# Performance work log

Measured on AMD Instinct MI355X. Metric: run time of the kernel, lower is better.

Reference implementation:

```python
import jax, jax.numpy as jnp
import numpy as np

H = 160; W = 160          # BEV grid
C = 256                   # embed_dims
NH = 8                    # num_heads
HD = C // NH              # head dim
NP = 4                    # num_points
LC = 2                    # max_num_levels == num agents for cross attn
Q = H * W                 # num queries = num values per level
EPS = 1e-5

def _lin(key, din, dout):
    k1, k2 = jax.random.split(key)
    s = float(1.0 / np.sqrt(din))
    return (jax.random.uniform(k1, (din, dout), jnp.float32, -s, s),
            jax.random.uniform(k2, (dout,), jnp.float32, -s, s))

def setup_inputs():
    ks = jax.random.split(jax.random.key(0), 16)
    inp = {
        "query": jax.random.normal(ks[0], (1, Q, C), jnp.float32),
        "query_pos": jax.random.normal(ks[1], (1, Q, C), jnp.float32),
        "value": jax.random.normal(ks[2], (LC, Q, C), jnp.float32),
        "ref_2d": jax.random.uniform(ks[3], (1, Q, LC, 2), jnp.float32),
        "spatial_shapes": jnp.full((LC, 2), H, dtype=jnp.int32),
    }
    i = 4
    for pre, L in (("sa", 1), ("ca", LC)):
        inp[pre + "_off_w"], inp[pre + "_off_b"] = _lin(ks[i], C, L * NH * NP * 2); i += 1
        inp[pre + "_aw_w"], inp[pre + "_aw_b"] = _lin(ks[i], C, L * NH * NP); i += 1
        inp[pre + "_vp_w"], inp[pre + "_vp_b"] = _lin(ks[i], C, C); i += 1
        inp[pre + "_op_w"], inp[pre + "_op_b"] = _lin(ks[i], C, C); i += 1
    inp["ffn_w1"], inp["ffn_b1"] = _lin(ks[i], C, 4 * C); i += 1
    inp["ffn_w2"], inp["ffn_b2"] = _lin(ks[i], 4 * C, C); i += 1
    for j in (1, 2, 3):
        inp["ln%d_g" % j] = jnp.ones((C,), jnp.float32)
        inp["ln%d_b" % j] = jnp.zeros((C,), jnp.float32)
    return inp

def _bilinear(val, x, y):
    # val: [NH, H*W, HD]; x, y: [NH, Q, NP] pixel coords
    # matches F.grid_sample(mode='bilinear', padding_mode='zeros', align_corners=False)
    x0 = jnp.floor(x); y0 = jnp.floor(y)
    def corner(xi, yi):
        valid = ((xi >= 0) & (xi < W) & (yi >= 0) & (yi < H))[..., None]
        idx = (jnp.clip(yi, 0, H - 1) * W + jnp.clip(xi, 0, W - 1)).astype(jnp.int32)
        return jax.vmap(lambda vh, ih: vh[ih])(val, idx) * valid  # [NH, Q, NP, HD]
    tx = (x - x0)[..., None]; ty = (y - y0)[..., None]
    top = corner(x0, y0) * (1 - tx) + corner(x0 + 1, y0) * tx
    bot = corner(x0, y0 + 1) * (1 - tx) + corner(x0 + 1, y0 + 1) * tx
    return top * (1 - ty) + bot * ty

def _defor_attn(q_in, query_pos, value, ref, spatial_shapes, p, L):
    # q_in [1,Q,C]; value [L,Q,C]; ref [1,Q,L,2] in [0,1]
    identity = q_in
    q = (q_in + query_pos)[0]                                   # [Q, C]
    v = value @ p["vp_w"] + p["vp_b"]
    v = v.reshape(L, Q, NH, HD).transpose(0, 2, 1, 3)           # [L, NH, HW, HD]
    off = (q @ p["off_w"] + p["off_b"]).reshape(Q, NH, L, NP, 2)
    aw = jax.nn.softmax((q @ p["aw_w"] + p["aw_b"]).reshape(Q, NH, L * NP), -1)
    aw = aw.reshape(Q, NH, L, NP)
    # offset_normalizer = [W_, H_] from spatial_shapes[0] (all levels share shape)
    norm = jnp.stack([spatial_shapes[0, 1], spatial_shapes[0, 0]]).astype(jnp.float32)
    loc = ref[0, :, None, :, None, :] + off / norm              # [Q, NH, L, NP, 2]
    x = jnp.transpose(loc[..., 0] * W - 0.5, (2, 1, 0, 3))      # [L, NH, Q, NP]
    y = jnp.transpose(loc[..., 1] * H - 0.5, (2, 1, 0, 3))
    sampled = jax.vmap(_bilinear)(v, x, y)                      # [L, NH, Q, NP, HD]
    out = jnp.einsum('lhqpd,qhlp->qhd', sampled, aw).reshape(1, Q, C)
    return out @ p["op_w"] + p["op_b"] + identity

def _ln(x, g, b):
    mu = jnp.mean(x, -1, keepdims=True)
    var = jnp.mean((x - mu) ** 2, -1, keepdims=True)
    return (x - mu) * jax.lax.rsqrt(var + EPS) * g + b

_DA_KEYS = ("off_w", "off_b", "aw_w", "aw_b", "vp_w", "vp_b", "op_w", "op_b")

def _block(query, query_pos, value, ref_2d, spatial_shapes, P):
    sa = {k: P["sa_" + k] for k in _DA_KEYS}
    ca = {k: P["ca_" + k] for k in _DA_KEYS}
    q = _defor_attn(query, query_pos, query, ref_2d[:, :, :1, :], spatial_shapes[:1], sa, 1)
    q = _ln(q, P["ln1_g"], P["ln1_b"])
    q = _defor_attn(q, query_pos, value, ref_2d, spatial_shapes[:1], ca, LC)
    q = _ln(q, P["ln2_g"], P["ln2_b"])
    q = q + (jax.nn.relu(q @ P["ffn_w1"] + P["ffn_b1"]) @ P["ffn_w2"] + P["ffn_b2"])
    q = _ln(q, P["ln3_g"], P["ln3_b"])
    return q

def reference(query, query_pos, value, ref_2d, spatial_shapes,
              sa_off_w, sa_off_b, sa_aw_w, sa_aw_b, sa_vp_w, sa_vp_b, sa_op_w, sa_op_b,
              ca_off_w, ca_off_b, ca_aw_w, ca_aw_b, ca_vp_w, ca_vp_b, ca_op_w, ca_op_b,
              ffn_w1, ffn_b1, ffn_w2, ffn_b2,
              ln1_g, ln1_b, ln2_g, ln2_b, ln3_g, ln3_b):
    P = dict(sa_off_w=sa_off_w, sa_off_b=sa_off_b, sa_aw_w=sa_aw_w, sa_aw_b=sa_aw_b,
             sa_vp_w=sa_vp_w, sa_vp_b=sa_vp_b, sa_op_w=sa_op_w, sa_op_b=sa_op_b,
             ca_off_w=ca_off_w, ca_off_b=ca_off_b, ca_aw_w=ca_aw_w, ca_aw_b=ca_aw_b,
             ca_vp_w=ca_vp_w, ca_vp_b=ca_vp_b, ca_op_w=ca_op_w, ca_op_b=ca_op_b,
             ffn_w1=ffn_w1, ffn_b1=ffn_b1, ffn_w2=ffn_w2, ffn_b2=ffn_b2,
             ln1_g=ln1_g, ln1_b=ln1_b, ln2_g=ln2_g, ln2_b=ln2_b, ln3_g=ln3_g, ln3_b=ln3_b)
    q = _block(query, query_pos, value, ref_2d, spatial_shapes, P)
    return (q, query_pos, value, ref_2d, spatial_shapes)
```

## Files before the change

### kernel.cpp

```cpp
#include <hip/hip_runtime.h>

#define Q_   25600
#define C_   256
#define NH_  8
#define HD_  32
#define NP_  4
#define LC_  2
#define HW_  160

#define QC   (Q_ * C_)
#define VC   (2 * QC)
#define REFN (Q_ * LC_ * 2)

typedef unsigned short ushort_t;
typedef __attribute__((ext_vector_type(8))) short short8;
typedef __attribute__((ext_vector_type(4))) float f32x4;

__device__ __forceinline__ float b2f(ushort_t u) {
    union { unsigned int u32; float f; } c; c.u32 = ((unsigned int)u) << 16; return c.f;
}
__device__ __forceinline__ ushort_t f2b(float f) {
    union { float f; unsigned int u32; } c; c.f = f;
    unsigned int u = c.u32;
    return (ushort_t)((u + 0x7FFFu + ((u >> 16) & 1u)) >> 16);
}
__device__ __forceinline__ unsigned int pack2(float lo, float hi){
    return (unsigned int)f2b(lo) | ((unsigned int)f2b(hi) << 16);
}
__device__ __forceinline__ short8 pack8(float4 a, float4 b){
    union { short8 s; ushort_t u[8]; } r;
    r.u[0]=f2b(a.x); r.u[1]=f2b(a.y); r.u[2]=f2b(a.z); r.u[3]=f2b(a.w);
    r.u[4]=f2b(b.x); r.u[5]=f2b(b.y); r.u[6]=f2b(b.z); r.u[7]=f2b(b.w);
    return r.s;
}

struct TDesc { const float* src; ushort_t* dst; int K; int N; };
struct TAll  { TDesc t[10]; };

#define QC4   (QC / 4)
#define TRANS_TOTAL 860160
#define PRO_TOTAL (QC4 + TRANS_TOTAL)

__global__ __launch_bounds__(256) void prologue_kernel(
    const float* __restrict__ query, const float* __restrict__ qpos,
    ushort_t* __restrict__ qpq, TAll td)
{
    int i = blockIdx.x * 256 + threadIdx.x;
    if (i < QC4) {
        float4 qv = ((const float4*)query)[i];
        float4 pv = ((const float4*)qpos)[i];
        uint2 o;
        o.x = pack2(qv.x + pv.x, qv.y + pv.y);
        o.y = pack2(qv.z + pv.z, qv.w + pv.w);
        ((uint2*)qpq)[i] = o;
        return;
    }
    i -= QC4;
    #pragma unroll 1
    for (int m = 0; m < 10; m++) {
        int sz = td.t[m].K * td.t[m].N;
        if (i < sz) {
            int N = td.t[m].N, K = td.t[m].K;
            int k = i / N, n = i - k * N;
            td.t[m].dst[(size_t)n * K + k] = f2b(td.t[m].src[i]);
            return;
        }
        i -= sz;
    }
}

__global__ void ss_kernel(const int* __restrict__ ss, float* __restrict__ out_ss)
{
    int i = threadIdx.x;
    if (i < 4) out_ss[i] = (float)ss[i];
}

template<int WN, bool RELU, int RESM, bool AF32>
__global__ __launch_bounds__(256) void gemm_bf16(
    const ushort_t* __restrict__ A16, const float* __restrict__ A32,
    const ushort_t* __restrict__ Bt, const float* __restrict__ bias,
    const ushort_t* __restrict__ res16, const float* __restrict__ res32,
    ushort_t* __restrict__ Cout, int M, int N, int K)
{
    const int lane = threadIdx.x & 63;
    const int wave = threadIdx.x >> 6;
    const int m0 = blockIdx.x * 256 + wave * 64;
    const int n0 = blockIdx.y * (16 * WN);
    const int r = lane & 15, quad = lane >> 4;

    f32x4 acc[4][WN];
    #pragma unroll
    for (int i = 0; i < 4; i++)
        #pragma unroll
        for (int j = 0; j < WN; j++) acc[i][j] = (f32x4){0.f, 0.f, 0.f, 0.f};

    const ushort_t* Ab16 = AF32 ? nullptr : (A16 + (size_t)(m0 + r) * K + quad * 8);
    const float*    Ab32 = AF32 ? (A32 + (size_t)(m0 + r) * K + quad * 8) : nullptr;
    const ushort_t* Bbase = Bt + (size_t)(n0 + r) * K + quad * 8;

    for (int k0 = 0; k0 < K; k0 += 32) {
        short8 af[4], bfr[WN];
        #pragma unroll
        for (int i = 0; i < 4; i++) {
            if (AF32) {
                float4 u = *(const float4*)(Ab32 + (size_t)i * 16 * K + k0);
                float4 v = *(const float4*)(Ab32 + (size_t)i * 16 * K + k0 + 4);
                af[i] = pack8(u, v);
            } else {
                af[i] = *(const short8*)(Ab16 + (size_t)i * 16 * K + k0);
            }
        }
        #pragma unroll
        for (int j = 0; j < WN; j++)
            bfr[j] = *(const short8*)(Bbase + (size_t)j * 16 * K + k0);
        #pragma unroll
        for (int i = 0; i < 4; i++)
            #pragma unroll
            for (int j = 0; j < WN; j++)
                acc[i][j] = __builtin_amdgcn_mfma_f32_16x16x32_bf16(af[i], bfr[j], acc[i][j], 0, 0, 0);
    }

    float bv[WN];
    #pragma unroll
    for (int j = 0; j < WN; j++) bv[j] = bias[n0 + j * 16 + r];

    #pragma unroll
    for (int i = 0; i < 4; i++) {
        int row = m0 + i * 16 + quad * 4;
        #pragma unroll
        for (int j = 0; j < WN; j++) {
            int col = n0 + j * 16 + r;
            #pragma unroll
            for (int t = 0; t < 4; t++) {
                float v = acc[i][j][t] + bv[j];
                if (RESM == 1) v += b2f(res16[(size_t)(row + t) * N + col]);
                if (RESM == 2) v += res32[(size_t)(row + t) * N + col];
                if (RELU) v = fmaxf(v, 0.f);
                Cout[(size_t)(row + t) * N + col] = f2b(v);
            }
        }
    }
}

template<int L>
__global__ __launch_bounds__(256) void sample_kernel(
    const ushort_t* __restrict__ v,
    const ushort_t* __restrict__ off,
    const ushort_t* __restrict__ aw,
    const float*    __restrict__ ref,
    ushort_t* __restrict__ outp)
{
    const int g = (blockIdx.x * 256 + threadIdx.x) >> 5;
    const int d = threadIdx.x & 31;
    const int q = g >> 3;
    const int h = g & 7;
    const int P = L * NP_;

    const ushort_t* awp = aw + (size_t)q * (NH_ * P) + h * P;
    float w[2 * NP_];
    float mx = -1e30f;
    #pragma unroll
    for (int i = 0; i < P; i++) { w[i] = b2f(awp[i]); mx = fmaxf(mx, w[i]); }
    float s = 0.f;
    #pragma unroll
    for (int i = 0; i < P; i++) { w[i] = __expf(w[i] - mx); s += w[i]; }
    const float inv = 1.f / s;

    const ushort_t* offp = off + (size_t)q * (NH_ * P * 2) + h * P * 2;
    float acc = 0.f;
    #pragma unroll
    for (int l = 0; l < L; l++) {
        float rx = ref[((size_t)q * LC_ + l) * 2 + 0] * (float)HW_ - 0.5f;
        float ry = ref[((size_t)q * LC_ + l) * 2 + 1] * (float)HW_ - 0.5f;
        const ushort_t* vl = v + (size_t)l * Q_ * C_ + h * HD_ + d;
        #pragma unroll
        for (int p = 0; p < NP_; p++) {
            int ip = l * NP_ + p;
            float x = rx + b2f(offp[ip * 2 + 0]);
            float y = ry + b2f(offp[ip * 2 + 1]);
            x = fminf(fmaxf(x, -1e4f), 1e4f);
            y = fminf(fmaxf(y, -1e4f), 1e4f);
            float xf = floorf(x), yf = floorf(y);
            float tx = x - xf, ty = y - yf;
            int x0 = (int)xf, y0 = (int)yf;

            float c00, c10, c01, c11;
            {
                int xc, yc; bool val;
                #define CORNER(OUT, XI, YI) \
                    xc = (XI) < 0 ? 0 : ((XI) > HW_-1 ? HW_-1 : (XI)); \
                    yc = (YI) < 0 ? 0 : ((YI) > HW_-1 ? HW_-1 : (YI)); \
                    val = ((XI) >= 0) & ((XI) < HW_) & ((YI) >= 0) & ((YI) < HW_); \
                    OUT = val ? b2f(vl[(size_t)(yc * HW_ + xc) * C_]) : 0.f;
                CORNER(c00, x0,     y0)
                CORNER(c10, x0 + 1, y0)
                CORNER(c01, x0,     y0 + 1)
                CORNER(c11, x0 + 1, y0 + 1)
                #undef CORNER
            }
            float bil = (c00 * (1.f - tx) + c10 * tx) * (1.f - ty)
                      + (c01 * (1.f - tx) + c11 * tx) * ty;
            acc += bil * (w[ip] * inv);
        }
    }
    outp[(size_t)q * C_ + h * HD_ + d] = f2b(acc);
}

template<bool OUT32>
__global__ __launch_bounds__(256) void ln_kernel(
    const ushort_t* __restrict__ x, const float* __restrict__ g,
    const float* __restrict__ b, ushort_t* __restrict__ y16,
    float* __restrict__ y32,
    const float* __restrict__ qpos, ushort_t* __restrict__ y2)
{
    const int lane = threadIdx.x & 63;
    const int wave = threadIdx.x >> 6;
    const size_t row = (size_t)blockIdx.x * 4 + wave;
    const size_t base = row * C_ + lane * 4;

    uint2 xv = *(const uint2*)(x + base);
    float f0 = b2f((ushort_t)(xv.x & 0xFFFF)), f1 = b2f((ushort_t)(xv.x >> 16));
    float f2 = b2f((ushort_t)(xv.y & 0xFFFF)), f3 = b2f((ushort_t)(xv.y >> 16));
    float s  = f0 + f1 + f2 + f3;
    float sq = f0 * f0 + f1 * f1 + f2 * f2 + f3 * f3;
    #pragma unroll
    for (int m = 1; m < 64; m <<= 1) { s += __shfl_xor(s, m, 64); sq += __shfl_xor(sq, m, 64); }
    float mean = s * (1.f / 256.f);
    float var  = sq * (1.f / 256.f) - mean * mean;
    float rinv = rsqrtf(fmaxf(var, 0.f) + 1e-5f);

    float4 gv = *(const float4*)(g + lane * 4);
    float4 bv = *(const float4*)(b + lane * 4);
    float o0 = (f0 - mean) * rinv * gv.x + bv.x;
    float o1 = (f1 - mean) * rinv * gv.y + bv.y;
    float o2 = (f2 - mean) * rinv * gv.z + bv.z;
    float o3 = (f3 - mean) * rinv * gv.w + bv.w;

    if (OUT32) {
        float4 o; o.x = o0; o.y = o1; o.z = o2; o.w = o3;
        *(float4*)(y32 + base) = o;
    } else {
        uint2 ov; ov.x = pack2(o0, o1); ov.y = pack2(o2, o3);
        *(uint2*)(y16 + base) = ov;
    }

    if (y2) {
        float4 pv = *(const float4*)(qpos + base);
        uint2 o2v;
        o2v.x = pack2(o0 + pv.x, o1 + pv.y);
        o2v.y = pack2(o2 + pv.z, o3 + pv.w);
        *(uint2*)(y2 + base) = o2v;
    }
}

extern "C" void kernel_launch(void* const* d_in, const int* in_sizes, int n_in,
                              void* d_out, int out_size, void* d_ws, size_t ws_size,
                              hipStream_t stream)
{
    const float* query = (const float*)d_in[0];
    const float* qpos  = (const float*)d_in[1];
    const float* value = (const float*)d_in[2];
    const float* ref   = (const float*)d_in[3];
    const int*   ss    = (const int*)d_in[4];
    const float* sa_off_w = (const float*)d_in[5];
    const float* sa_off_b = (const float*)d_in[6];
    const float* sa_aw_w  = (const float*)d_in[7];
    const float* sa_aw_b  = (const float*)d_in[8];
    const float* sa_vp_w  = (const float*)d_in[9];
    const float* sa_vp_b  = (const float*)d_in[10];
    const float* sa_op_w  = (const float*)d_in[11];
    const float* sa_op_b  = (const float*)d_in[12];
    const float* ca_off_w = (const float*)d_in[13];
    const float* ca_off_b = (const float*)d_in[14];
    const float* ca_aw_w  = (const float*)d_in[15];
    const float* ca_aw_b  = (const float*)d_in[16];
    const float* ca_vp_w  = (const float*)d_in[17];
    const float* ca_vp_b  = (const float*)d_in[18];
    const float* ca_op_w  = (const float*)d_in[19];
    const float* ca_op_b  = (const float*)d_in[20];
    const float* ffn_w1   = (const float*)d_in[21];
    const float* ffn_b1   = (const float*)d_in[22];
    const float* ffn_w2   = (const float*)d_in[23];
    const float* ffn_b2   = (const float*)d_in[24];
    const float* ln1_g = (const float*)d_in[25];
    const float* ln1_b = (const float*)d_in[26];
    const float* ln2_g = (const float*)d_in[27];
    const float* ln2_b = (const float*)d_in[28];
    const float* ln3_g = (const float*)d_in[29];
    const float* ln3_b = (const float*)d_in[30];

    float* outf    = (float*)d_out;
    float* out_q   = outf;
    float* out_qp  = outf + QC;
    float* out_val = outf + 2 * (size_t)QC;
    float* out_ref = outf + 4 * (size_t)QC;
    float* out_ss  = outf + 4 * (size_t)QC + REFN;

    ushort_t* dsc    = (ushort_t*)d_out;
    ushort_t* vbuf   = dsc;
    ushort_t* tmp    = dsc + 2 * (size_t)QC;
    ushort_t* offb   = dsc + 3 * (size_t)QC;
    ushort_t* awb    = dsc + 3 * (size_t)QC + (size_t)Q_ * 128;
    ushort_t* hidden = dsc;

    char* base = (char*)d_ws;
    size_t offbyte = 0;
    auto alloc = [&](size_t elems) -> ushort_t* {
        ushort_t* p = (ushort_t*)(base + offbyte);
        offbyte += ((elems * 2 + 255) / 256) * 256;
        return p;
    };
    ushort_t* wt_sa_off = alloc(256 * 64);
    ushort_t* wt_sa_aw  = alloc(256 * 32);
    ushort_t* wt_sa_vp  = alloc(256 * 256);
    ushort_t* wt_sa_op  = alloc(256 * 256);
    ushort_t* wt_ca_off = alloc(256 * 128);
    ushort_t* wt_ca_aw  = alloc(256 * 64);
    ushort_t* wt_ca_vp  = alloc(256 * 256);
    ushort_t* wt_ca_op  = alloc(256 * 256);
    ushort_t* wt_ffn1   = alloc(256 * 1024);
    ushort_t* wt_ffn2   = alloc(1024 * 256);
    ushort_t* qpq  = alloc(QC);
    ushort_t* attn = alloc(QC);
    ushort_t* q1   = alloc(QC);
    ushort_t* q2   = attn;

    TAll td;
    const float* srcs[10] = {sa_off_w, sa_aw_w, sa_vp_w, sa_op_w, ca_off_w,
                             ca_aw_w, ca_vp_w, ca_op_w, ffn_w1, ffn_w2};
    ushort_t* dsts[10] = {wt_sa_off, wt_sa_aw, wt_sa_vp, wt_sa_op, wt_ca_off,
                          wt_ca_aw, wt_ca_vp, wt_ca_op, wt_ffn1, wt_ffn2};
    int Ks[10] = {256, 256, 256, 256, 256, 256, 256, 256, 256, 1024};
    int Ns[10] = {64, 32, 256, 256, 128, 64, 256, 256, 1024, 256};
    for (int m = 0; m < 10; m++) { td.t[m] = {srcs[m], dsts[m], Ks[m], Ns[m]}; }

    prologue_kernel<<<(PRO_TOTAL + 255) / 256, 256, 0, stream>>>(query, qpos, qpq, td);

    gemm_bf16<4, false, 0, true><<<dim3(Q_ / 256, 4), 256, 0, stream>>>(
        nullptr, query, wt_sa_vp, sa_vp_b, nullptr, nullptr, vbuf, Q_, 256, 256);
    gemm_bf16<4, false, 0, false><<<dim3(Q_ / 256, 1), 256, 0, stream>>>(
        qpq, nullptr, wt_sa_off, sa_off_b, nullptr, nullptr, offb, Q_, 64, 256);
    gemm_bf16<2, false, 0, false><<<dim3(Q_ / 256, 1), 256, 0, stream>>>(
        qpq, nullptr, wt_sa_aw, sa_aw_b, nullptr, nullptr, awb, Q_, 32, 256);
    sample_kernel<1><<<(Q_ * NH_) / 8, 256, 0, stream>>>(vbuf, offb, awb, ref, attn);
    gemm_bf16<4, false, 2, false><<<dim3(Q_ / 256, 4), 256, 0, stream>>>(
        attn, nullptr, wt_sa_op, sa_op_b, nullptr, query, tmp, Q_, 256, 256);
    ln_kernel<false><<<Q_ / 4, 256, 0, stream>>>(tmp, ln1_g, ln1_b, q1, nullptr, qpos, qpq);

    gemm_bf16<4, false, 0, true><<<dim3(2 * Q_ / 256, 4), 256, 0, stream>>>(
        nullptr, value, wt_ca_vp, ca_vp_b, nullptr, nullptr, vbuf, 2 * Q_, 256, 256);
    gemm_bf16<4, false, 0, false><<<dim3(Q_ / 256, 2), 256, 0, stream>>>(
        qpq, nullptr, wt_ca_off, ca_off_b, nullptr, nullptr, offb, Q_, 128, 256);
    gemm_bf16<4, false, 0, false><<<dim3(Q_ / 256, 1), 256, 0, stream>>>(
        qpq, nullptr, wt_ca_aw, ca_aw_b, nullptr, nullptr, awb, Q_, 64, 256);
    sample_kernel<2><<<(Q_ * NH_) / 8, 256, 0, stream>>>(vbuf, offb, awb, ref, attn);
    gemm_bf16<4, false, 1, false><<<dim3(Q_ / 256, 4), 256, 0, stream>>>(
        attn, nullptr, wt_ca_op, ca_op_b, q1, nullptr, tmp, Q_, 256, 256);
    ln_kernel<false><<<Q_ / 4, 256, 0, stream>>>(tmp, ln2_g, ln2_b, q2, nullptr, nullptr, nullptr);

    gemm_bf16<4, true, 0, false><<<dim3(Q_ / 256, 16), 256, 0, stream>>>(
        q2, nullptr, wt_ffn1, ffn_b1, nullptr, nullptr, hidden, Q_, 1024, 256);
    gemm_bf16<4, false, 1, false><<<dim3(Q_ / 256, 4), 256, 0, stream>>>(
        hidden, nullptr, wt_ffn2, ffn_b2, q2, nullptr, q1, Q_, 256, 1024);
    ln_kernel<true><<<Q_ / 4, 256, 0, stream>>>(q1, ln3_g, ln3_b, nullptr, out_q, nullptr, nullptr);

    hipMemcpyAsync(out_qp,  qpos,  (size_t)QC * 4,  hipMemcpyDeviceToDevice, stream);
    hipMemcpyAsync(out_val, value, (size_t)VC * 4,  hipMemcpyDeviceToDevice, stream);
    hipMemcpyAsync(out_ref, ref,   (size_t)REFN * 4, hipMemcpyDeviceToDevice, stream);
    ss_kernel<<<1, 64, 0, stream>>>(ss, out_ss);

    (void)in_sizes; (void)n_in; (void)out_size; (void)ws_size;
}
```

Before: 906.3 us.

## Use head-major value layout, two groups per thread in sampler, fuse passthrough copies

The value-projection GEMM now writes its output in a [level][head][pixel][headdim] layout, so each bilinear corner gather in the sampler reads a compact 64-byte row instead of striding across the full channel dimension. The sampler handles two (query, head) groups per thread with vectorized loads of offsets, weights and reference points, which raises memory-level parallelism and halves the grid. The passthrough copies of ref and value are folded into the sampler kernels in place of separate memcpy calls, so they overlap with the gather work. The cost is more registers per thread and a scattered store pattern in the GEMM epilogue.

```diff
diff --git a/kernel.cpp b/kernel.cpp
--- a/kernel.cpp
+++ b/kernel.cpp
@@ -75,7 +75,7 @@
     if (i < 4) out_ss[i] = (float)ss[i];
 }
 
-template<int WN, bool RELU, int RESM, bool AF32>
+template<int WN, bool RELU, int RESM, bool AF32, int OSPLIT>
 __global__ __launch_bounds__(256) void gemm_bf16(
     const ushort_t* __restrict__ A16, const float* __restrict__ A32,
     const ushort_t* __restrict__ Bt, const float* __restrict__ bias,
@@ -126,17 +126,25 @@
 
     #pragma unroll
     for (int i = 0; i < 4; i++) {
-        int row = m0 + i * 16 + quad * 4;
+        int row0 = m0 + i * 16 + quad * 4;
         #pragma unroll
         for (int j = 0; j < WN; j++) {
             int col = n0 + j * 16 + r;
             #pragma unroll
             for (int t = 0; t < 4; t++) {
+                int row = row0 + t;
                 float v = acc[i][j][t] + bv[j];
-                if (RESM == 1) v += b2f(res16[(size_t)(row + t) * N + col]);
-                if (RESM == 2) v += res32[(size_t)(row + t) * N + col];
+                if (RESM == 1) v += b2f(res16[(size_t)row * N + col]);
+                if (RESM == 2) v += res32[(size_t)row * N + col];
                 if (RELU) v = fmaxf(v, 0.f);
-                Cout[(size_t)(row + t) * N + col] = f2b(v);
+                if (OSPLIT) {
+                    int l = row / Q_;
+                    int pix = row - l * Q_;
+                    int h = col >> 5, dd = col & 31;
+                    Cout[(((size_t)l * NH_ + h) * (size_t)Q_ + pix) * HD_ + dd] = f2b(v);
+                } else {
+                    Cout[(size_t)row * N + col] = f2b(v);
+                }
             }
         }
     }
@@ -148,62 +156,113 @@
     const ushort_t* __restrict__ off,
     const ushort_t* __restrict__ aw,
     const float*    __restrict__ ref,
-    ushort_t* __restrict__ outp)
-{
-    const int g = (blockIdx.x * 256 + threadIdx.x) >> 5;
+    ushort_t* __restrict__ outp,
+    const float4* __restrict__ csrc, float4* __restrict__ cdst, int cnum)
+{
+    const int tid = blockIdx.x * 256 + threadIdx.x;
+    const bool do_copy = (tid < cnum);
+    float4 cval;
+    if (do_copy) cval = csrc[tid];
+
+    constexpr int P = L * NP_;
+    constexpr int HALFG = Q_ * NH_ / 2;
+    const int g0 = tid >> 5;
     const int d = threadIdx.x & 31;
-    const int q = g >> 3;
-    const int h = g & 7;
-    const int P = L * NP_;
-
-    const ushort_t* awp = aw + (size_t)q * (NH_ * P) + h * P;
-    float w[2 * NP_];
-    float mx = -1e30f;
-    #pragma unroll
-    for (int i = 0; i < P; i++) { w[i] = b2f(awp[i]); mx = fmaxf(mx, w[i]); }
-    float s = 0.f;
-    #pragma unroll
-    for (int i = 0; i < P; i++) { w[i] = __expf(w[i] - mx); s += w[i]; }
-    const float inv = 1.f / s;
-
-    const ushort_t* offp = off + (size_t)q * (NH_ * P * 2) + h * P * 2;
-    float acc = 0.f;
+
+    int qq[2], hh[2];
+    float wn[2][P];
+    ushort_t offr[2][2 * P];
+    float rx[2][L], ry[2][L];
+
+    #pragma unroll
+    for (int u = 0; u < 2; u++) {
+        const int g = g0 + u * HALFG;
+        const int q = g >> 3, h = g & 7;
+        qq[u] = q; hh[u] = h;
+
+        ushort_t awr[P];
+        const ushort_t* awp = aw + (size_t)q * (NH_ * P) + h * P;
+        if (L == 2) {
+            union { uint4 v4; ushort_t us[8]; } t; t.v4 = *(const uint4*)awp;
+            #pragma unroll
+            for (int i = 0; i < 8; i++) awr[i] = t.us[i];
+        } else {
+            union { uint2 v2; ushort_t us[4]; } t; t.v2 = *(const uint2*)awp;
+            #pragma unroll
+            for (int i = 0; i < 4; i++) awr[i] = t.us[i];
+        }
+        const ushort_t* offp = off + (size_t)q * (NH_ * 2 * P) + h * 2 * P;
+        if (L == 2) {
+            union { uint4 v4; ushort_t us[8]; } t0, t1;
+            t0.v4 = ((const uint4*)offp)[0];
+            t1.v4 = ((const uint4*)offp)[1];
+            #pragma unroll
+            for (int i = 0; i < 8; i++) { offr[u][i] = t0.us[i]; offr[u][8 + i] = t1.us[i]; }
+        } else {
+            union { uint4 v4; ushort_t us[8]; } t0;
+            t0.v4 = *(const uint4*)offp;
+            #pragma unroll
+            for (int i = 0; i < 8; i++) offr[u][i] = t0.us[i];
+        }
+        float w[P]; float mx = -1e30f;
+        #pragma unroll
+        for (int i = 0; i < P; i++) { w[i] = b2f(awr[i]); mx = fmaxf(mx, w[i]); }
+        float s = 0.f;
+        #pragma unroll
+        for (int i = 0; i < P; i++) { w[i] = __expf(w[i] - mx); s += w[i]; }
+        float inv = 1.f / s;
+        #pragma unroll
+        for (int i = 0; i < P; i++) wn[u][i] = w[i] * inv;
+        if (L == 2) {
+            float4 r4 = *(const float4*)(ref + (size_t)q * 4);
+            rx[u][0] = r4.x * (float)HW_ - 0.5f; ry[u][0] = r4.y * (float)HW_ - 0.5f;
+            rx[u][1] = r4.z * (float)HW_ - 0.5f; ry[u][1] = r4.w * (float)HW_ - 0.5f;
+        } else {
+            float2 r2 = *(const float2*)(ref + (size_t)q * 4);
+            rx[u][0] = r2.x * (float)HW_ - 0.5f; ry[u][0] = r2.y * (float)HW_ - 0.5f;
+        }
+    }
+
+    float acc[2] = {0.f, 0.f};
     #pragma unroll
     for (int l = 0; l < L; l++) {
-        float rx = ref[((size_t)q * LC_ + l) * 2 + 0] * (float)HW_ - 0.5f;
-        float ry = ref[((size_t)q * LC_ + l) * 2 + 1] * (float)HW_ - 0.5f;
-        const ushort_t* vl = v + (size_t)l * Q_ * C_ + h * HD_ + d;
         #pragma unroll
         for (int p = 0; p < NP_; p++) {
-            int ip = l * NP_ + p;
-            float x = rx + b2f(offp[ip * 2 + 0]);
-            float y = ry + b2f(offp[ip * 2 + 1]);
-            x = fminf(fmaxf(x, -1e4f), 1e4f);
-            y = fminf(fmaxf(y, -1e4f), 1e4f);
-            float xf = floorf(x), yf = floorf(y);
-            float tx = x - xf, ty = y - yf;
-            int x0 = (int)xf, y0 = (int)yf;
-
-            float c00, c10, c01, c11;
-            {
+            const int ip = l * NP_ + p;
+            float c[2][4], tx[2], ty[2];
+            #pragma unroll
+            for (int u = 0; u < 2; u++) {
+                float x = rx[u][l] + b2f(offr[u][ip * 2 + 0]);
+                float y = ry[u][l] + b2f(offr[u][ip * 2 + 1]);
+                x = fminf(fmaxf(x, -1e4f), 1e4f);
+                y = fminf(fmaxf(y, -1e4f), 1e4f);
+                float xf = floorf(x), yf = floorf(y);
+                tx[u] = x - xf; ty[u] = y - yf;
+                int x0 = (int)xf, y0 = (int)yf;
+                const ushort_t* base = v + ((size_t)(l * NH_ + hh[u]) * (size_t)Q_) * HD_ + d;
                 int xc, yc; bool val;
                 #define CORNER(OUT, XI, YI) \
                     xc = (XI) < 0 ? 0 : ((XI) > HW_-1 ? HW_-1 : (XI)); \
                     yc = (YI) < 0 ? 0 : ((YI) > HW_-1 ? HW_-1 : (YI)); \
                     val = ((XI) >= 0) & ((XI) < HW_) & ((YI) >= 0) & ((YI) < HW_); \
-                    OUT = val ? b2f(vl[(size_t)(yc * HW_ + xc) * C_]) : 0.f;
-                CORNER(c00, x0,     y0)
-                CORNER(c10, x0 + 1, y0)
-                CORNER(c01, x0,     y0 + 1)
-                CORNER(c11, x0 + 1, y0 + 1)
+                    OUT = val ? b2f(base[(size_t)(yc * HW_ + xc) * HD_]) : 0.f;
+                CORNER(c[u][0], x0,     y0)
+                CORNER(c[u][1], x0 + 1, y0)
+                CORNER(c[u][2], x0,     y0 + 1)
+                CORNER(c[u][3], x0 + 1, y0 + 1)
                 #undef CORNER
             }
-            float bil = (c00 * (1.f - tx) + c10 * tx) * (1.f - ty)
-                      + (c01 * (1.f - tx) + c11 * tx) * ty;
-            acc += bil * (w[ip] * inv);
-        }
-    }
-    outp[(size_t)q * C_ + h * HD_ + d] = f2b(acc);
+            #pragma unroll
+            for (int u = 0; u < 2; u++) {
+                float bil = (c[u][0] * (1.f - tx[u]) + c[u][1] * tx[u]) * (1.f - ty[u])
+                          + (c[u][2] * (1.f - tx[u]) + c[u][3] * tx[u]) * ty[u];
+                acc[u] += bil * wn[u][ip];
+            }
+        }
+    }
+    outp[(size_t)qq[0] * C_ + hh[0] * HD_ + d] = f2b(acc[0]);
+    outp[(size_t)qq[1] * C_ + hh[1] * HD_ + d] = f2b(acc[1]);
+    if (do_copy) cdst[tid] = cval;
 }
 
 template<bool OUT32>
@@ -336,37 +395,39 @@
 
     prologue_kernel<<<(PRO_TOTAL + 255) / 256, 256, 0, stream>>>(query, qpos, qpq, td);
 
-    gemm_bf16<4, false, 0, true><<<dim3(Q_ / 256, 4), 256, 0, stream>>>(
+    gemm_bf16<4, false, 0, true, 1><<<dim3(Q_ / 256, 4), 256, 0, stream>>>(
         nullptr, query, wt_sa_vp, sa_vp_b, nullptr, nullptr, vbuf, Q_, 256, 256);
-    gemm_bf16<4, false, 0, false><<<dim3(Q_ / 256, 1), 256, 0, stream>>>(
+    gemm_bf16<4, false, 0, false, 0><<<dim3(Q_ / 256, 1), 256, 0, stream>>>(
         qpq, nullptr, wt_sa_off, sa_off_b, nullptr, nullptr, offb, Q_, 64, 256);
-    gemm_bf16<2, false, 0, false><<<dim3(Q_ / 256, 1), 256, 0, stream>>>(
+    gemm_bf16<2, false, 0, false, 0><<<dim3(Q_ / 256, 1), 256, 0, stream>>>(
         qpq, nullptr, wt_sa_aw, sa_aw_b, nullptr, nullptr, awb, Q_, 32, 256);
-    sample_kernel<1><<<(Q_ * NH_) / 8, 256, 0, stream>>>(vbuf, offb, awb, ref, attn);
-    gemm_bf16<4, false, 2, false><<<dim3(Q_ / 256, 4), 256, 0, stream>>>(
+    sample_kernel<1><<<(Q_ * NH_) / 16, 256, 0, stream>>>(
+        vbuf, offb, awb, ref, attn,
+        (const float4*)ref, (float4*)out_ref, REFN / 4);
+    gemm_bf16<4, false, 2, false, 0><<<dim3(Q_ / 256, 4), 256, 0, stream>>>(
         attn, nullptr, wt_sa_op, sa_op_b, nullptr, query, tmp, Q_, 256, 256);
     ln_kernel<false><<<Q_ / 4, 256, 0, stream>>>(tmp, ln1_g, ln1_b, q1, nullptr, qpos, qpq);
 
-    gemm_bf16<4, false, 0, true><<<dim3(2 * Q_ / 256, 4), 256, 0, stream>>>(
+    gemm_bf16<4, false, 0, true, 1><<<dim3(2 * Q_ / 256, 4), 256, 0, stream>>>(
         nullptr, value, wt_ca_vp, ca_vp_b, nullptr, nullptr, vbuf, 2 * Q_, 256, 256);
-    gemm_bf16<4, false, 0, false><<<dim3(Q_ / 256, 2), 256, 0, stream>>>(
+    gemm_bf16<4, false, 0, false, 0><<<dim3(Q_ / 256, 2), 256, 0, stream>>>(
         qpq, nullptr, wt_ca_off, ca_off_b, nullptr, nullptr, offb, Q_, 128, 256);
-    gemm_bf16<4, false, 0, false><<<dim3(Q_ / 256, 1), 256, 0, stream>>>(
+    gemm_bf16<4, false, 0, false, 0><<<dim3(Q_ / 256, 1), 256, 0, stream>>>(
         qpq, nullptr, wt_ca_aw, ca_aw_b, nullptr, nullptr, awb, Q_, 64, 256);
-    sample_kernel<2><<<(Q_ * NH_) / 8, 256, 0, stream>>>(vbuf, offb, awb, ref, attn);
-    gemm_bf16<4, false, 1, false><<<dim3(Q_ / 256, 4), 256, 0, stream>>>(
+    sample_kernel<2><<<(Q_ * NH_) / 16, 256, 0, stream>>>(
+        vbuf, offb, awb, ref, attn,
+        (const float4*)value, (float4*)out_val, VC / 4);
+    gemm_bf16<4, false, 1, false, 0><<<dim3(Q_ / 256, 4), 256, 0, stream>>>(
         attn, nullptr, wt_ca_op, ca_op_b, q1, nullptr, tmp, Q_, 256, 256);
     ln_kernel<false><<<Q_ / 4, 256, 0, stream>>>(tmp, ln2_g, ln2_b, q2, nullptr, nullptr, nullptr);
 
-    gemm_bf16<4, true, 0, false><<<dim3(Q_ / 256, 16), 256, 0, stream>>>(
+    gemm_bf16<4, true, 0, false, 0><<<dim3(Q_ / 256, 16), 256, 0, stream>>>(
         q2, nullptr, wt_ffn1, ffn_b1, nullptr, nullptr, hidden, Q_, 1024, 256);
-    gemm_bf16<4, false, 1, false><<<dim3(Q_ / 256, 4), 256, 0, stream>>>(
+    gemm_bf16<4, false, 1, false, 0><<<dim3(Q_ / 256, 4), 256, 0, stream>>>(
         hidden, nullptr, wt_ffn2, ffn_b2, q2, nullptr, q1, Q_, 256, 1024);
     ln_kernel<true><<<Q_ / 4, 256, 0, stream>>>(q1, ln3_g, ln3_b, nullptr, out_q, nullptr, nullptr);
 
-    hipMemcpyAsync(out_qp,  qpos,  (size_t)QC * 4,  hipMemcpyDeviceToDevice, stream);
-    hipMemcpyAsync(out_val, value, (size_t)VC * 4,  hipMemcpyDeviceToDevice, stream);
-    hipMemcpyAsync(out_ref, ref,   (size_t)REFN * 4, hipMemcpyDeviceToDevice, stream);
+    hipMemcpyAsync(out_qp, qpos, (size_t)QC * 4, hipMemcpyDeviceToDevice, stream);
     ss_kernel<<<1, 64, 0, stream>>>(ss, out_ss);
 
     (void)in_sizes; (void)n_in; (void)out_size; (void)ws_size;
```

After: 1.038 ms. +14.5%, slower.
